# Kernel optimization log

Hardware: AMD Instinct MI355X
Metric: run time of the kernel (lower is better)

The kernel has to match this reference:

```python
import jax, jax.numpy as jnp
import numpy as np

C = 256       # in_channels
A = 6         # act_dim
B = 10000     # number of graphs (batch)
N = B * A     # total nodes
E = 960000    # number of edges
H = 32        # hidden_size


def setup_inputs() -> dict:
    key = jax.random.key(0)
    ks = jax.random.split(key, 20)
    s = 1.0 / np.sqrt(C)
    inp = {
        "state": jax.random.normal(ks[0], (N, C), jnp.float32),
        "edge_index": jax.random.randint(ks[1], (2, E), 0, N, jnp.int32),
        "action": jax.random.uniform(ks[2], (B, A), jnp.float32),
    }
    # GCNConv params (weight [C,C], bias [C]); conv4/conv5 exist but are unused by forward
    for i in range(5):
        inp[f"W{i+1}"] = jax.random.normal(ks[3 + i], (C, C), jnp.float32) * s
        inp[f"b{i+1}"] = jnp.zeros((C,), jnp.float32)
    D1 = 6 * C + 1
    inp["lin1_w"] = jax.random.normal(ks[10], (D1, H), jnp.float32) / np.sqrt(D1)
    inp["lin1_b"] = jnp.zeros((H,), jnp.float32)
    inp["lin2_w"] = jax.random.normal(ks[11], (H, H), jnp.float32) / np.sqrt(H)
    inp["lin2_b"] = jnp.zeros((H,), jnp.float32)
    inp["lin3_w"] = jax.random.normal(ks[12], (H, 1), jnp.float32) / np.sqrt(H)
    inp["lin3_b"] = jnp.zeros((1,), jnp.float32)
    return inp


def _gcn(x, W, b, src, dst, dinv):
    # PyG GCNConv: xW, then D^{-1/2}(A+I)D^{-1/2} aggregation, then bias.
    xw = x @ W                                    # [N, C]
    norm = dinv[src] * dinv[dst]                  # [E]
    agg = jax.ops.segment_sum(xw[src] * norm[:, None], dst, num_segments=N)
    agg = agg + xw * (dinv * dinv)[:, None]       # self-loop term
    return agg + b


def reference(state, edge_index, action,
              W1, b1, W2, b2, W3, b3, W4, b4, W5, b5,
              lin1_w, lin1_b, lin2_w, lin2_b, lin3_w, lin3_b):
    src, dst = edge_index[0], edge_index[1]
    # degree of A + I, computed at destination nodes (gcn_norm with self-loops)
    deg = jax.ops.segment_sum(jnp.ones((E,), state.dtype), dst, num_segments=N) + 1.0
    dinv = jax.lax.rsqrt(deg)

    o1 = jax.nn.relu(_gcn(state, W1, b1, src, dst, dinv))
    o2 = jax.nn.relu(_gcn(o1, W2, b2, src, dst, dinv))
    o3 = jax.nn.relu(_gcn(o2, W3, b3, src, dst, dinv))
    # NOTE: original forward reuses conv3 for layers 4 and 5 (replicated faithfully)
    o4 = jax.nn.relu(_gcn(o3, W3, b3, src, dst, dinv))
    o5 = jax.nn.relu(_gcn(o4, W3, b3, src, dst, dinv))

    r = lambda t: t.reshape(-1, A, C)             # [B, A, C]
    concat = jnp.concatenate(
        [r(o1), r(o2), r(o3), r(o4), r(o5), r(state), action[..., None]], axis=-1)
    x = jax.nn.relu(concat @ lin1_w + lin1_b)     # [B, A, H]
    x = jax.nn.relu(x @ lin2_w + lin2_b)
    x = jnp.sum(x, axis=1)                        # readout over act_dim
    x = (x @ lin3_w + lin3_b).squeeze(-1)         # [B]
    return x
```

## Files before the change

kernel.cpp:

```cpp
#include <hip/hip_runtime.h>
#include <hip/hip_fp16.h>

#define NNODES 60000
#define NEDGES 960000
#define NGRAPH 10000

struct __align__(16) H8 { __half2 h[4]; };
struct __align__(8)  H4 { __half2 h[2]; };

typedef _Float16 f16x8 __attribute__((ext_vector_type(8)));
typedef float f32x4 __attribute__((ext_vector_type(4)));

#define LDA 264


__global__ void count_deg_k(const int* __restrict__ ei, int* __restrict__ deg) {
  int e = blockIdx.x * blockDim.x + threadIdx.x;
  atomicAdd(&deg[ei[NEDGES + e]], 1);
}

__global__ void scan1_k(const int* __restrict__ deg, int* __restrict__ rs,
                        int* __restrict__ bsum, float* __restrict__ dinv) {
  __shared__ int s[256];
  int tid = threadIdx.x;
  int i = blockIdx.x * 256 + tid;
  int v = (i < NNODES) ? deg[i] : 0;
  if (i < NNODES) dinv[i] = rsqrtf((float)v + 1.0f);
  int x = v;
  s[tid] = x; __syncthreads();
  #pragma unroll
  for (int off = 1; off < 256; off <<= 1) {
    int t = (tid >= off) ? s[tid - off] : 0;
    __syncthreads();
    x += t; s[tid] = x; __syncthreads();
  }
  if (i < NNODES) rs[i] = x - v;
  if (tid == 255) bsum[blockIdx.x] = x;
}

__global__ void scan2_k(int* __restrict__ bsum, int nb) {
  __shared__ int s[256];
  int tid = threadIdx.x;
  int v = (tid < nb) ? bsum[tid] : 0;
  int x = v; s[tid] = x; __syncthreads();
  #pragma unroll
  for (int off = 1; off < 256; off <<= 1) {
    int t = (tid >= off) ? s[tid - off] : 0;
    __syncthreads();
    x += t; s[tid] = x; __syncthreads();
  }
  if (tid < nb) bsum[tid] = x - v;
}

__global__ void scan3_k(int* __restrict__ rs, const int* __restrict__ bsum) {
  int i = blockIdx.x * 256 + threadIdx.x;
  if (i < NNODES) rs[i] += bsum[blockIdx.x];
  if (i == 0) rs[NNODES] = NEDGES;
}

__global__ void scatter_k(const int* __restrict__ ei, const int* __restrict__ rs,
                          int* __restrict__ cursor, unsigned short* __restrict__ csr) {
  int e = blockIdx.x * blockDim.x + threadIdx.x;
  int s = ei[e], d = ei[NEDGES + e];
  int pos = rs[d] + atomicAdd(&cursor[d], 1);
  csr[pos] = (unsigned short)s;
}


__global__ void wpack_k(const float* __restrict__ W1, const float* __restrict__ W2,
                        const float* __restrict__ W3, __half* __restrict__ B1,
                        __half* __restrict__ B2, __half* __restrict__ B3) {
  int which = blockIdx.x >> 7;
  int c = blockIdx.x & 127;
  const float* W = which == 0 ? W1 : (which == 1 ? W2 : W3);
  __half* Bp = which == 0 ? B1 : (which == 1 ? B2 : B3);
  int kq = c >> 4, wcf = c & 15;
  int t = threadIdx.x;
  int l = t >> 2;
  int j0 = (t & 3) * 2;
  int li = l & 15, lg = l >> 4;
  int n = wcf * 16 + li;
  int k = kq * 32 + lg * 8 + j0;
  __half2 v;
  v.x = __float2half_rn(W[(size_t)k * 256 + n]);
  v.y = __float2half_rn(W[(size_t)(k + 1) * 256 + n]);
  *reinterpret_cast<__half2*>(Bp + (size_t)c * 512 + 2 * t) = v;
}

__global__ void lwpack_k(const float* __restrict__ l1w, __half* __restrict__ Pp) {
  int b = blockIdx.x;
  int l = b >> 4, cp = b & 15;
  int kq = cp >> 1, hh = cp & 1;
  int t = threadIdx.x;
  int ln = t >> 2;
  int j0 = (t & 3) * 2;
  int li = ln & 15, lg = ln >> 4;
  int dim = hh * 16 + li;
  int k = kq * 32 + lg * 8 + j0;
  __half2 v;
  v.x = __float2half_rn(l1w[((size_t)l * 256 + k) * 32 + dim]);
  v.y = __float2half_rn(l1w[((size_t)l * 256 + k + 1) * 32 + dim]);
  *reinterpret_cast<__half2*>(Pp + (size_t)b * 512 + 2 * t) = v;
}


__device__ __forceinline__ void gemm_body32(
    _Float16 (*As)[LDA], int m0, int nh, int tid,
    const __half* __restrict__ Bp, const __half* __restrict__ Pp,
    const float* __restrict__ dinv, __half* __restrict__ Y,
    float* __restrict__ part) {
  const int lane = tid & 63;
  const int wid = tid >> 6;
  const int wr2 = wid >> 1, wcl = wid & 1;
  const int li = lane & 15, lg = lane >> 4;

  f32x4 acc[4];
  #pragma unroll
  for (int j = 0; j < 4; ++j) acc[j] = (f32x4){0.f, 0.f, 0.f, 0.f};
  f32x4 p = (f32x4){0.f, 0.f, 0.f, 0.f};

  const __half* bwave = Bp + (size_t)(nh * 8 + wcl * 4) * 512 + lane * 8;
  const __half* pbase = Pp + (size_t)wcl * 512 + lane * 8;

  #pragma unroll
  for (int kq = 0; kq < 8; ++kq) {
    int k0 = kq * 32;
    f16x8 a = *reinterpret_cast<const f16x8*>(&As[wr2 * 16 + li][k0 + lg * 8]);
    f16x8 b0 = *reinterpret_cast<const f16x8*>(bwave + ((size_t)kq * 16 + 0) * 512);
    f16x8 b1 = *reinterpret_cast<const f16x8*>(bwave + ((size_t)kq * 16 + 1) * 512);
    f16x8 b2 = *reinterpret_cast<const f16x8*>(bwave + ((size_t)kq * 16 + 2) * 512);
    f16x8 b3 = *reinterpret_cast<const f16x8*>(bwave + ((size_t)kq * 16 + 3) * 512);
    acc[0] = __builtin_amdgcn_mfma_f32_16x16x32_f16(b0, a, acc[0], 0, 0, 0);
    acc[1] = __builtin_amdgcn_mfma_f32_16x16x32_f16(b1, a, acc[1], 0, 0, 0);
    acc[2] = __builtin_amdgcn_mfma_f32_16x16x32_f16(b2, a, acc[2], 0, 0, 0);
    acc[3] = __builtin_amdgcn_mfma_f32_16x16x32_f16(b3, a, acc[3], 0, 0, 0);
    if (nh == 0) {
      f16x8 bp = *reinterpret_cast<const f16x8*>(pbase + (size_t)kq * 2 * 512);
      p = __builtin_amdgcn_mfma_f32_16x16x32_f16(bp, a, p, 0, 0, 0);
    }
  }

  __syncthreads();

  {
    int row = wr2 * 16 + li;
    int r = m0 + row;
    float dv = dinv[r];
    #pragma unroll
    for (int cf = 0; cf < 4; ++cf) {
      int col = wcl * 64 + cf * 16 + lg * 4;
      H4 o;
      o.h[0].x = __float2half_rn(acc[cf][0] * dv);
      o.h[0].y = __float2half_rn(acc[cf][1] * dv);
      o.h[1].x = __float2half_rn(acc[cf][2] * dv);
      o.h[1].y = __float2half_rn(acc[cf][3] * dv);
      *reinterpret_cast<H4*>(&As[row][col]) = o;
    }
    if (nh == 0) {
      float4 v;
      v.x = p[0]; v.y = p[1]; v.z = p[2]; v.w = p[3];
      *reinterpret_cast<float4*>(part + (size_t)r * 32 + wcl * 16 + lg * 4) = v;
    }
  }

  __syncthreads();

  #pragma unroll
  for (int l = 0; l < 2; ++l) {
    int f = l * 256 + tid;
    int row = f >> 4, c8 = (f & 15) * 8;
    *reinterpret_cast<H8*>(Y + (size_t)(m0 + row) * 256 + nh * 128 + c8) =
        *reinterpret_cast<const H8*>(&As[row][c8]);
  }
}


__launch_bounds__(256, 6)
__global__ void gemm0_k(const float* __restrict__ Xf, const __half* __restrict__ Bp,
                        const float* __restrict__ dinv, __half* __restrict__ Y,
                        const __half* __restrict__ Pp, float* __restrict__ part) {
  __shared__ _Float16 As[32][LDA];
  const int tid = threadIdx.x;
  const int m0 = (blockIdx.x >> 1) * 32;
  const int nh = blockIdx.x & 1;
  #pragma unroll
  for (int l = 0; l < 4; ++l) {
    int f = l * 256 + tid;
    int row = f >> 5, c8 = (f & 31) * 8;
    const float* src = Xf + (size_t)(m0 + row) * 256 + c8;
    float4 u = *reinterpret_cast<const float4*>(src);
    float4 v = *reinterpret_cast<const float4*>(src + 4);
    H8 o;
    o.h[0].x = __float2half_rn(u.x); o.h[0].y = __float2half_rn(u.y);
    o.h[1].x = __float2half_rn(u.z); o.h[1].y = __float2half_rn(u.w);
    o.h[2].x = __float2half_rn(v.x); o.h[2].y = __float2half_rn(v.y);
    o.h[3].x = __float2half_rn(v.z); o.h[3].y = __float2half_rn(v.w);
    *reinterpret_cast<H8*>(&As[row][c8]) = o;
  }
  __syncthreads();
  gemm_body32(As, m0, nh, tid, Bp, Pp, dinv, Y, part);
}


__launch_bounds__(256, 6)
__global__ void gemm_k(const __half* __restrict__ Xh, const __half* __restrict__ Bp,
                       const float* __restrict__ dinv, __half* __restrict__ Y,
                       const __half* __restrict__ Pp, float* __restrict__ part) {
  __shared__ _Float16 As[32][LDA];
  const int tid = threadIdx.x;
  const int m0 = (blockIdx.x >> 1) * 32;
  const int nh = blockIdx.x & 1;
  #pragma unroll
  for (int l = 0; l < 4; ++l) {
    int f = l * 256 + tid;
    int row = f >> 5, c8 = (f & 31) * 8;
    *reinterpret_cast<H8*>(&As[row][c8]) =
        *reinterpret_cast<const H8*>(Xh + (size_t)(m0 + row) * 256 + c8);
  }
  __syncthreads();
  gemm_body32(As, m0, nh, tid, Bp, Pp, dinv, Y, part);
}


__launch_bounds__(256, 4)
__global__ void proj_k(const __half* __restrict__ Xh, const __half* __restrict__ Pp,
                       float* __restrict__ part) {
  __shared__ _Float16 As[64][LDA];
  const int tid = threadIdx.x;
  const int m0 = blockIdx.x * 64;
  #pragma unroll
  for (int l = 0; l < 8; ++l) {
    int f = l * 256 + tid;
    int row = f >> 5, c8 = (f & 31) * 8;
    *reinterpret_cast<H8*>(&As[row][c8]) =
        *reinterpret_cast<const H8*>(Xh + (size_t)(m0 + row) * 256 + c8);
  }
  __syncthreads();

  const int lane = tid & 63;
  const int wid = tid >> 6;
  const int li = lane & 15, lg = lane >> 4;
  const __half* pbase = Pp + lane * 8;

  f32x4 p0 = (f32x4){0.f, 0.f, 0.f, 0.f};
  f32x4 p1 = (f32x4){0.f, 0.f, 0.f, 0.f};
  #pragma unroll
  for (int kq = 0; kq < 8; ++kq) {
    int k0 = kq * 32;
    f16x8 ap = *reinterpret_cast<const f16x8*>(&As[wid * 16 + li][k0 + lg * 8]);
    f16x8 bp0 = *reinterpret_cast<const f16x8*>(pbase + ((size_t)kq * 2 + 0) * 512);
    f16x8 bp1 = *reinterpret_cast<const f16x8*>(pbase + ((size_t)kq * 2 + 1) * 512);
    p0 = __builtin_amdgcn_mfma_f32_16x16x32_f16(bp0, ap, p0, 0, 0, 0);
    p1 = __builtin_amdgcn_mfma_f32_16x16x32_f16(bp1, ap, p1, 0, 0, 0);
  }
  int pr = m0 + wid * 16 + li;
  {
    float4 v0, v1;
    v0.x = p0[0]; v0.y = p0[1]; v0.z = p0[2]; v0.w = p0[3];
    v1.x = p1[0]; v1.y = p1[1]; v1.z = p1[2]; v1.w = p1[3];
    *reinterpret_cast<float4*>(part + (size_t)pr * 32 + lg * 4) = v0;
    *reinterpret_cast<float4*>(part + (size_t)pr * 32 + 16 + lg * 4) = v1;
  }
}


__device__ inline void addH8(float* acc, const H8& v) {
  #pragma unroll
  for (int q = 0; q < 4; ++q) {
    acc[q * 2 + 0] += __low2float(v.h[q]);
    acc[q * 2 + 1] += __high2float(v.h[q]);
  }
}

__global__ void gather_k(const __half* __restrict__ ysh, const int* __restrict__ rs,
                         const unsigned short* __restrict__ csr, const float* __restrict__ dinv,
                         const float* __restrict__ bias, __half* __restrict__ out) {
  int tid = threadIdx.x;
  int lane = tid & 63;
  int wave = (blockIdx.x * blockDim.x + tid) >> 6;
  int d = wave * 2 + (lane >> 5);
  int c8 = (lane & 31) * 8;

  float acc[8];
  H8 self = *reinterpret_cast<const H8*>(ysh + (size_t)d * 256 + c8);
  #pragma unroll
  for (int q = 0; q < 4; ++q) {
    acc[q * 2 + 0] = __low2float(self.h[q]);
    acc[q * 2 + 1] = __high2float(self.h[q]);
  }

  int e = rs[d], end = rs[d + 1];
  for (; e + 3 < end; e += 4) {
    int s0 = csr[e], s1 = csr[e + 1], s2 = csr[e + 2], s3 = csr[e + 3];
    H8 v0 = *reinterpret_cast<const H8*>(ysh + (size_t)s0 * 256 + c8);
    H8 v1 = *reinterpret_cast<const H8*>(ysh + (size_t)s1 * 256 + c8);
    H8 v2 = *reinterpret_cast<const H8*>(ysh + (size_t)s2 * 256 + c8);
    H8 v3 = *reinterpret_cast<const H8*>(ysh + (size_t)s3 * 256 + c8);
    addH8(acc, v0);
    addH8(acc, v1);
    addH8(acc, v2);
    addH8(acc, v3);
  }
  for (; e < end; ++e) {
    int s0 = csr[e];
    H8 v0 = *reinterpret_cast<const H8*>(ysh + (size_t)s0 * 256 + c8);
    addH8(acc, v0);
  }

  float dv = dinv[d];
  float4 b0 = *reinterpret_cast<const float4*>(bias + c8);
  float4 b1 = *reinterpret_cast<const float4*>(bias + c8 + 4);
  float r0 = fmaxf(acc[0] * dv + b0.x, 0.f);
  float r1 = fmaxf(acc[1] * dv + b0.y, 0.f);
  float r2 = fmaxf(acc[2] * dv + b0.z, 0.f);
  float r3 = fmaxf(acc[3] * dv + b0.w, 0.f);
  float r4 = fmaxf(acc[4] * dv + b1.x, 0.f);
  float r5 = fmaxf(acc[5] * dv + b1.y, 0.f);
  float r6 = fmaxf(acc[6] * dv + b1.z, 0.f);
  float r7 = fmaxf(acc[7] * dv + b1.w, 0.f);
  H8 o;
  o.h[0].x = __float2half_rn(r0); o.h[0].y = __float2half_rn(r1);
  o.h[1].x = __float2half_rn(r2); o.h[1].y = __float2half_rn(r3);
  o.h[2].x = __float2half_rn(r4); o.h[2].y = __float2half_rn(r5);
  o.h[3].x = __float2half_rn(r6); o.h[3].y = __float2half_rn(r7);
  *reinterpret_cast<H8*>(out + (size_t)d * 256 + c8) = o;
}


__launch_bounds__(192)
__global__ void mlpfinal_k(const float* __restrict__ p0, const float* __restrict__ p1,
                           const float* __restrict__ p2, const float* __restrict__ p3,
                           const float* __restrict__ p4, const float* __restrict__ p5,
                           const float* __restrict__ action, const float* __restrict__ l1wlast,
                           const float* __restrict__ l1b, const float* __restrict__ l2w,
                           const float* __restrict__ l2b, const float* __restrict__ l3w,
                           const float* __restrict__ l3b, float* __restrict__ out) {
  __shared__ float w2s[1024];
  __shared__ float h1s[6][33];
  __shared__ float red[3];
  int tid = threadIdx.x;
  for (int i = tid; i < 1024; i += 192) w2s[i] = l2w[i];
  int a = tid >> 5, dim = tid & 31;
  int n = blockIdx.x * 6 + a;
  int idx = n * 32 + dim;
  float h1 = l1b[dim] + action[n] * l1wlast[dim]
           + p0[idx] + p1[idx] + p2[idx] + p3[idx] + p4[idx] + p5[idx];
  h1s[a][dim] = fmaxf(h1, 0.f);
  __syncthreads();
  float acc = l2b[dim];
  #pragma unroll
  for (int k = 0; k < 32; ++k) acc += h1s[a][k] * w2s[k * 32 + dim];
  float v = fmaxf(acc, 0.f) * l3w[dim];
  #pragma unroll
  for (int off = 32; off; off >>= 1) v += __shfl_down(v, off, 64);
  int lane = tid & 63, wave = tid >> 6;
  if (lane == 0) red[wave] = v;
  __syncthreads();
  if (tid == 0) out[blockIdx.x] = red[0] + red[1] + red[2] + l3b[0];
}


extern "C" void kernel_launch(void* const* d_in, const int* in_sizes, int n_in,
                              void* d_out, int out_size, void* d_ws, size_t ws_size,
                              hipStream_t stream) {
  const float* state  = (const float*)d_in[0];
  const int*   ei     = (const int*)d_in[1];
  const float* action = (const float*)d_in[2];
  const float* W1 = (const float*)d_in[3];
  const float* b1 = (const float*)d_in[4];
  const float* W2 = (const float*)d_in[5];
  const float* b2 = (const float*)d_in[6];
  const float* W3 = (const float*)d_in[7];
  const float* b3 = (const float*)d_in[8];
  const float* l1w = (const float*)d_in[13];
  const float* l1b = (const float*)d_in[14];
  const float* l2w = (const float*)d_in[15];
  const float* l2b = (const float*)d_in[16];
  const float* l3w = (const float*)d_in[17];
  const float* l3b = (const float*)d_in[18];
  float* out = (float*)d_out;

  char* base = (char*)d_ws;
  size_t off = 0;
  auto carve = [&](size_t bytes) {
    char* q = base + off;
    off += (bytes + 255) & ~(size_t)255;
    return q;
  };
  __half* ysh   = (__half*)carve((size_t)NNODES * 256 * 2);
  __half* obufh = (__half*)carve((size_t)NNODES * 256 * 2);
  __half* Bp1   = (__half*)carve(128 * 512 * 2);
  __half* Bp2   = (__half*)carve(128 * 512 * 2);
  __half* Bp3   = (__half*)carve(128 * 512 * 2);
  __half* Pp    = (__half*)carve(96 * 512 * 2);
  float* parts[6];
  for (int i = 0; i < 6; ++i) parts[i] = (float*)carve((size_t)NNODES * 32 * 4);
  float* dinv  = (float*)carve(NNODES * 4);
  char*  zbase = (char*)carve(0);
  int*   deg   = (int*)carve(NNODES * 4);
  int*   cursor= (int*)carve(NNODES * 4);
  size_t zlen  = (size_t)((char*)carve(0) - zbase);
  int*   rs    = (int*)carve((NNODES + 1) * 4);
  unsigned short* csr = (unsigned short*)carve((size_t)NEDGES * 2);
  int*   bsum  = (int*)carve(256 * 4);

  hipMemsetAsync(zbase, 0, zlen, stream);

  wpack_k<<<128 * 3, 256, 0, stream>>>(W1, W2, W3, Bp1, Bp2, Bp3);
  lwpack_k<<<96, 256, 0, stream>>>(l1w, Pp);

  count_deg_k<<<NEDGES / 256, 256, 0, stream>>>(ei, deg);
  int nb = (NNODES + 255) / 256;
  scan1_k<<<nb, 256, 0, stream>>>(deg, rs, bsum, dinv);
  scan2_k<<<1, 256, 0, stream>>>(bsum, nb);
  scan3_k<<<nb, 256, 0, stream>>>(rs, bsum);
  scatter_k<<<NEDGES / 256, 256, 0, stream>>>(ei, rs, cursor, csr);

  int gblocks = (NNODES / 32) * 2;
  const __half* Bps[5] = {Bp1, Bp2, Bp3, Bp3, Bp3};
  const float*  bs[5]  = {b1, b2, b3, b3, b3};

  gemm0_k<<<gblocks, 256, 0, stream>>>(state, Bp1, dinv, ysh,
                                       Pp + (size_t)5 * 16 * 512, parts[5]);
  for (int layer = 1; layer < 5; ++layer) {
    gather_k<<<NNODES / 8, 256, 0, stream>>>(ysh, rs, csr, dinv, bs[layer - 1], obufh);
    gemm_k<<<gblocks, 256, 0, stream>>>(obufh, Bps[layer], dinv, ysh,
                                        Pp + (size_t)(layer - 1) * 16 * 512, parts[layer - 1]);
  }
  gather_k<<<NNODES / 8, 256, 0, stream>>>(ysh, rs, csr, dinv, b3, obufh);
  proj_k<<<NNODES / 64, 256, 0, stream>>>(obufh, Pp + (size_t)4 * 16 * 512, parts[4]);

  mlpfinal_k<<<NGRAPH, 192, 0, stream>>>(parts[0], parts[1], parts[2], parts[3], parts[4],
                                         parts[5], action, l1w + 1536 * 32, l1b, l2w, l2b,
                                         l3w, l3b, out);
}
```

Baseline: 642.2 us.

## Compute full 256-wide GEMM per block, fuse prep kernels, fold last projection into MLP

Each GEMM block now computes all 256 output columns for its 32 rows instead of splitting the columns across two blocks. This halves the A-tile loads and removes the duplicate projection branch, at the cost of more accumulator registers and lower occupancy. The weight-packing kernels and the memset are merged into one prep kernel that also zeroes the degree and cursor arrays. The separate proj_k launch is removed, and the layer-5 projection is computed inside mlpfinal_k as a scalar dot product over fp16 o5 read from global memory, which trades an MFMA kernel for per-thread scalar FMAs.

New measurement: 653.6 us. Within noise of the previous version (+1.8%).

```diff
diff --git a/kernel.cpp b/kernel.cpp
--- a/kernel.cpp
+++ b/kernel.cpp
@@ -67,45 +67,50 @@
 }
 
 
-__global__ void wpack_k(const float* __restrict__ W1, const float* __restrict__ W2,
-                        const float* __restrict__ W3, __half* __restrict__ B1,
-                        __half* __restrict__ B2, __half* __restrict__ B3) {
-  int which = blockIdx.x >> 7;
-  int c = blockIdx.x & 127;
-  const float* W = which == 0 ? W1 : (which == 1 ? W2 : W3);
-  __half* Bp = which == 0 ? B1 : (which == 1 ? B2 : B3);
-  int kq = c >> 4, wcf = c & 15;
+__global__ void prep_k(const float* __restrict__ W1, const float* __restrict__ W2,
+                       const float* __restrict__ W3, const float* __restrict__ l1w,
+                       __half* __restrict__ B1, __half* __restrict__ B2,
+                       __half* __restrict__ B3, __half* __restrict__ Pp,
+                       int* __restrict__ deg, int* __restrict__ cursor) {
+  int bid = blockIdx.x;
   int t = threadIdx.x;
-  int l = t >> 2;
-  int j0 = (t & 3) * 2;
-  int li = l & 15, lg = l >> 4;
-  int n = wcf * 16 + li;
-  int k = kq * 32 + lg * 8 + j0;
-  __half2 v;
-  v.x = __float2half_rn(W[(size_t)k * 256 + n]);
-  v.y = __float2half_rn(W[(size_t)(k + 1) * 256 + n]);
-  *reinterpret_cast<__half2*>(Bp + (size_t)c * 512 + 2 * t) = v;
-}
-
-__global__ void lwpack_k(const float* __restrict__ l1w, __half* __restrict__ Pp) {
-  int b = blockIdx.x;
-  int l = b >> 4, cp = b & 15;
-  int kq = cp >> 1, hh = cp & 1;
-  int t = threadIdx.x;
-  int ln = t >> 2;
-  int j0 = (t & 3) * 2;
-  int li = ln & 15, lg = ln >> 4;
-  int dim = hh * 16 + li;
-  int k = kq * 32 + lg * 8 + j0;
-  __half2 v;
-  v.x = __float2half_rn(l1w[((size_t)l * 256 + k) * 32 + dim]);
-  v.y = __float2half_rn(l1w[((size_t)l * 256 + k + 1) * 32 + dim]);
-  *reinterpret_cast<__half2*>(Pp + (size_t)b * 512 + 2 * t) = v;
-}
-
-
-__device__ __forceinline__ void gemm_body32(
-    _Float16 (*As)[LDA], int m0, int nh, int tid,
+  if (bid < 384) {
+    int which = bid >> 7;
+    int c = bid & 127;
+    const float* W = which == 0 ? W1 : (which == 1 ? W2 : W3);
+    __half* Bp = which == 0 ? B1 : (which == 1 ? B2 : B3);
+    int kq = c >> 4, wcf = c & 15;
+    int l = t >> 2;
+    int j0 = (t & 3) * 2;
+    int li = l & 15, lg = l >> 4;
+    int n = wcf * 16 + li;
+    int k = kq * 32 + lg * 8 + j0;
+    __half2 v;
+    v.x = __float2half_rn(W[(size_t)k * 256 + n]);
+    v.y = __float2half_rn(W[(size_t)(k + 1) * 256 + n]);
+    *reinterpret_cast<__half2*>(Bp + (size_t)c * 512 + 2 * t) = v;
+  } else {
+    int b = bid - 384;
+    int l = b >> 4, cp = b & 15;
+    int kq = cp >> 1, hh = cp & 1;
+    int ln = t >> 2;
+    int j0 = (t & 3) * 2;
+    int li = ln & 15, lg = ln >> 4;
+    int dim = hh * 16 + li;
+    int k = kq * 32 + lg * 8 + j0;
+    __half2 v;
+    v.x = __float2half_rn(l1w[((size_t)l * 256 + k) * 32 + dim]);
+    v.y = __float2half_rn(l1w[((size_t)l * 256 + k + 1) * 32 + dim]);
+    *reinterpret_cast<__half2*>(Pp + (size_t)b * 512 + 2 * t) = v;
+  }
+  int z = bid * 256 + t;
+  if (z < NNODES) deg[z] = 0;
+  else if (z < 2 * NNODES) cursor[z - NNODES] = 0;
+}
+
+
+__device__ __forceinline__ void gemm_body256(
+    _Float16 (*As)[LDA], int m0, int tid,
     const __half* __restrict__ Bp, const __half* __restrict__ Pp,
     const float* __restrict__ dinv, __half* __restrict__ Y,
     float* __restrict__ part) {
@@ -114,27 +119,38 @@
   const int wr2 = wid >> 1, wcl = wid & 1;
   const int li = lane & 15, lg = lane >> 4;
 
-  f32x4 acc[4];
-  #pragma unroll
-  for (int j = 0; j < 4; ++j) acc[j] = (f32x4){0.f, 0.f, 0.f, 0.f};
+  f32x4 acc[8];
+  #pragma unroll
+  for (int j = 0; j < 8; ++j) acc[j] = (f32x4){0.f, 0.f, 0.f, 0.f};
   f32x4 p = (f32x4){0.f, 0.f, 0.f, 0.f};
 
-  const __half* bwave = Bp + (size_t)(nh * 8 + wcl * 4) * 512 + lane * 8;
+  const __half* bwave = Bp + (size_t)(wcl * 8) * 512 + lane * 8;
   const __half* pbase = Pp + (size_t)wcl * 512 + lane * 8;
 
   #pragma unroll
   for (int kq = 0; kq < 8; ++kq) {
-    int k0 = kq * 32;
-    f16x8 a = *reinterpret_cast<const f16x8*>(&As[wr2 * 16 + li][k0 + lg * 8]);
-    f16x8 b0 = *reinterpret_cast<const f16x8*>(bwave + ((size_t)kq * 16 + 0) * 512);
-    f16x8 b1 = *reinterpret_cast<const f16x8*>(bwave + ((size_t)kq * 16 + 1) * 512);
-    f16x8 b2 = *reinterpret_cast<const f16x8*>(bwave + ((size_t)kq * 16 + 2) * 512);
-    f16x8 b3 = *reinterpret_cast<const f16x8*>(bwave + ((size_t)kq * 16 + 3) * 512);
-    acc[0] = __builtin_amdgcn_mfma_f32_16x16x32_f16(b0, a, acc[0], 0, 0, 0);
-    acc[1] = __builtin_amdgcn_mfma_f32_16x16x32_f16(b1, a, acc[1], 0, 0, 0);
-    acc[2] = __builtin_amdgcn_mfma_f32_16x16x32_f16(b2, a, acc[2], 0, 0, 0);
-    acc[3] = __builtin_amdgcn_mfma_f32_16x16x32_f16(b3, a, acc[3], 0, 0, 0);
-    if (nh == 0) {
+    f16x8 a = *reinterpret_cast<const f16x8*>(&As[wr2 * 16 + li][kq * 32 + lg * 8]);
+    {
+      f16x8 b0 = *reinterpret_cast<const f16x8*>(bwave + ((size_t)kq * 16 + 0) * 512);
+      f16x8 b1 = *reinterpret_cast<const f16x8*>(bwave + ((size_t)kq * 16 + 1) * 512);
+      f16x8 b2 = *reinterpret_cast<const f16x8*>(bwave + ((size_t)kq * 16 + 2) * 512);
+      f16x8 b3 = *reinterpret_cast<const f16x8*>(bwave + ((size_t)kq * 16 + 3) * 512);
+      acc[0] = __builtin_amdgcn_mfma_f32_16x16x32_f16(b0, a, acc[0], 0, 0, 0);
+      acc[1] = __builtin_amdgcn_mfma_f32_16x16x32_f16(b1, a, acc[1], 0, 0, 0);
+      acc[2] = __builtin_amdgcn_mfma_f32_16x16x32_f16(b2, a, acc[2], 0, 0, 0);
+      acc[3] = __builtin_amdgcn_mfma_f32_16x16x32_f16(b3, a, acc[3], 0, 0, 0);
+    }
+    {
+      f16x8 b4 = *reinterpret_cast<const f16x8*>(bwave + ((size_t)kq * 16 + 4) * 512);
+      f16x8 b5 = *reinterpret_cast<const f16x8*>(bwave + ((size_t)kq * 16 + 5) * 512);
+      f16x8 b6 = *reinterpret_cast<const f16x8*>(bwave + ((size_t)kq * 16 + 6) * 512);
+      f16x8 b7 = *reinterpret_cast<const f16x8*>(bwave + ((size_t)kq * 16 + 7) * 512);
+      acc[4] = __builtin_amdgcn_mfma_f32_16x16x32_f16(b4, a, acc[4], 0, 0, 0);
+      acc[5] = __builtin_amdgcn_mfma_f32_16x16x32_f16(b5, a, acc[5], 0, 0, 0);
+      acc[6] = __builtin_amdgcn_mfma_f32_16x16x32_f16(b6, a, acc[6], 0, 0, 0);
+      acc[7] = __builtin_amdgcn_mfma_f32_16x16x32_f16(b7, a, acc[7], 0, 0, 0);
+    }
+    {
       f16x8 bp = *reinterpret_cast<const f16x8*>(pbase + (size_t)kq * 2 * 512);
       p = __builtin_amdgcn_mfma_f32_16x16x32_f16(bp, a, p, 0, 0, 0);
     }
@@ -147,8 +163,8 @@
     int r = m0 + row;
     float dv = dinv[r];
     #pragma unroll
-    for (int cf = 0; cf < 4; ++cf) {
-      int col = wcl * 64 + cf * 16 + lg * 4;
+    for (int cf = 0; cf < 8; ++cf) {
+      int col = wcl * 128 + cf * 16 + lg * 4;
       H4 o;
       o.h[0].x = __float2half_rn(acc[cf][0] * dv);
       o.h[0].y = __float2half_rn(acc[cf][1] * dv);
@@ -156,33 +172,30 @@
       o.h[1].y = __float2half_rn(acc[cf][3] * dv);
       *reinterpret_cast<H4*>(&As[row][col]) = o;
     }
-    if (nh == 0) {
-      float4 v;
-      v.x = p[0]; v.y = p[1]; v.z = p[2]; v.w = p[3];
-      *reinterpret_cast<float4*>(part + (size_t)r * 32 + wcl * 16 + lg * 4) = v;
-    }
-  }
-
-  __syncthreads();
-
-  #pragma unroll
-  for (int l = 0; l < 2; ++l) {
+    float4 v;
+    v.x = p[0]; v.y = p[1]; v.z = p[2]; v.w = p[3];
+    *reinterpret_cast<float4*>(part + (size_t)r * 32 + wcl * 16 + lg * 4) = v;
+  }
+
+  __syncthreads();
+
+  #pragma unroll
+  for (int l = 0; l < 4; ++l) {
     int f = l * 256 + tid;
-    int row = f >> 4, c8 = (f & 15) * 8;
-    *reinterpret_cast<H8*>(Y + (size_t)(m0 + row) * 256 + nh * 128 + c8) =
+    int row = f >> 5, c8 = (f & 31) * 8;
+    *reinterpret_cast<H8*>(Y + (size_t)(m0 + row) * 256 + c8) =
         *reinterpret_cast<const H8*>(&As[row][c8]);
   }
 }
 
 
-__launch_bounds__(256, 6)
+__launch_bounds__(256, 5)
 __global__ void gemm0_k(const float* __restrict__ Xf, const __half* __restrict__ Bp,
                         const float* __restrict__ dinv, __half* __restrict__ Y,
                         const __half* __restrict__ Pp, float* __restrict__ part) {
   __shared__ _Float16 As[32][LDA];
   const int tid = threadIdx.x;
-  const int m0 = (blockIdx.x >> 1) * 32;
-  const int nh = blockIdx.x & 1;
+  const int m0 = blockIdx.x * 32;
   #pragma unroll
   for (int l = 0; l < 4; ++l) {
     int f = l * 256 + tid;
@@ -198,18 +211,17 @@
     *reinterpret_cast<H8*>(&As[row][c8]) = o;
   }
   __syncthreads();
-  gemm_body32(As, m0, nh, tid, Bp, Pp, dinv, Y, part);
-}
-
-
-__launch_bounds__(256, 6)
+  gemm_body256(As, m0, tid, Bp, Pp, dinv, Y, part);
+}
+
+
+__launch_bounds__(256, 5)
 __global__ void gemm_k(const __half* __restrict__ Xh, const __half* __restrict__ Bp,
                        const float* __restrict__ dinv, __half* __restrict__ Y,
                        const __half* __restrict__ Pp, float* __restrict__ part) {
   __shared__ _Float16 As[32][LDA];
   const int tid = threadIdx.x;
-  const int m0 = (blockIdx.x >> 1) * 32;
-  const int nh = blockIdx.x & 1;
+  const int m0 = blockIdx.x * 32;
   #pragma unroll
   for (int l = 0; l < 4; ++l) {
     int f = l * 256 + tid;
@@ -218,49 +230,7 @@
         *reinterpret_cast<const H8*>(Xh + (size_t)(m0 + row) * 256 + c8);
   }
   __syncthreads();
-  gemm_body32(As, m0, nh, tid, Bp, Pp, dinv, Y, part);
-}
-
-
-__launch_bounds__(256, 4)
-__global__ void proj_k(const __half* __restrict__ Xh, const __half* __restrict__ Pp,
-                       float* __restrict__ part) {
-  __shared__ _Float16 As[64][LDA];
-  const int tid = threadIdx.x;
-  const int m0 = blockIdx.x * 64;
-  #pragma unroll
-  for (int l = 0; l < 8; ++l) {
-    int f = l * 256 + tid;
-    int row = f >> 5, c8 = (f & 31) * 8;
-    *reinterpret_cast<H8*>(&As[row][c8]) =
-        *reinterpret_cast<const H8*>(Xh + (size_t)(m0 + row) * 256 + c8);
-  }
-  __syncthreads();
-
-  const int lane = tid & 63;
-  const int wid = tid >> 6;
-  const int li = lane & 15, lg = lane >> 4;
-  const __half* pbase = Pp + lane * 8;
-
-  f32x4 p0 = (f32x4){0.f, 0.f, 0.f, 0.f};
-  f32x4 p1 = (f32x4){0.f, 0.f, 0.f, 0.f};
-  #pragma unroll
-  for (int kq = 0; kq < 8; ++kq) {
-    int k0 = kq * 32;
-    f16x8 ap = *reinterpret_cast<const f16x8*>(&As[wid * 16 + li][k0 + lg * 8]);
-    f16x8 bp0 = *reinterpret_cast<const f16x8*>(pbase + ((size_t)kq * 2 + 0) * 512);
-    f16x8 bp1 = *reinterpret_cast<const f16x8*>(pbase + ((size_t)kq * 2 + 1) * 512);
-    p0 = __builtin_amdgcn_mfma_f32_16x16x32_f16(bp0, ap, p0, 0, 0, 0);
-    p1 = __builtin_amdgcn_mfma_f32_16x16x32_f16(bp1, ap, p1, 0, 0, 0);
-  }
-  int pr = m0 + wid * 16 + li;
-  {
-    float4 v0, v1;
-    v0.x = p0[0]; v0.y = p0[1]; v0.z = p0[2]; v0.w = p0[3];
-    v1.x = p1[0]; v1.y = p1[1]; v1.z = p1[2]; v1.w = p1[3];
-    *reinterpret_cast<float4*>(part + (size_t)pr * 32 + lg * 4) = v0;
-    *reinterpret_cast<float4*>(part + (size_t)pr * 32 + 16 + lg * 4) = v1;
-  }
+  gemm_body256(As, m0, tid, Bp, Pp, dinv, Y, part);
 }
 
 
@@ -330,21 +300,33 @@
 __launch_bounds__(192)
 __global__ void mlpfinal_k(const float* __restrict__ p0, const float* __restrict__ p1,
                            const float* __restrict__ p2, const float* __restrict__ p3,
-                           const float* __restrict__ p4, const float* __restrict__ p5,
+                           const float* __restrict__ p5, const __half* __restrict__ o5h,
+                           const float* __restrict__ lw4,
                            const float* __restrict__ action, const float* __restrict__ l1wlast,
                            const float* __restrict__ l1b, const float* __restrict__ l2w,
                            const float* __restrict__ l2b, const float* __restrict__ l3w,
                            const float* __restrict__ l3b, float* __restrict__ out) {
   __shared__ float w2s[1024];
+  __shared__ __half o5s[6][256];
   __shared__ float h1s[6][33];
   __shared__ float red[3];
   int tid = threadIdx.x;
   for (int i = tid; i < 1024; i += 192) w2s[i] = l2w[i];
+  {
+    int row = tid >> 5, c8 = (tid & 31) * 8;
+    *reinterpret_cast<H8*>(&o5s[row][c8]) =
+        *reinterpret_cast<const H8*>(o5h + ((size_t)blockIdx.x * 6 + row) * 256 + c8);
+  }
+  __syncthreads();
   int a = tid >> 5, dim = tid & 31;
   int n = blockIdx.x * 6 + a;
   int idx = n * 32 + dim;
+  float p4 = 0.f;
+  #pragma unroll 8
+  for (int k = 0; k < 256; ++k)
+    p4 += __half2float(o5s[a][k]) * lw4[k * 32 + dim];
   float h1 = l1b[dim] + action[n] * l1wlast[dim]
-           + p0[idx] + p1[idx] + p2[idx] + p3[idx] + p4[idx] + p5[idx];
+           + p0[idx] + p1[idx] + p2[idx] + p3[idx] + p4 + p5[idx];
   h1s[a][dim] = fmaxf(h1, 0.f);
   __syncthreads();
   float acc = l2b[dim];
@@ -396,18 +378,13 @@
   float* parts[6];
   for (int i = 0; i < 6; ++i) parts[i] = (float*)carve((size_t)NNODES * 32 * 4);
   float* dinv  = (float*)carve(NNODES * 4);
-  char*  zbase = (char*)carve(0);
   int*   deg   = (int*)carve(NNODES * 4);
   int*   cursor= (int*)carve(NNODES * 4);
-  size_t zlen  = (size_t)((char*)carve(0) - zbase);
   int*   rs    = (int*)carve((NNODES + 1) * 4);
   unsigned short* csr = (unsigned short*)carve((size_t)NEDGES * 2);
   int*   bsum  = (int*)carve(256 * 4);
 
-  hipMemsetAsync(zbase, 0, zlen, stream);
-
-  wpack_k<<<128 * 3, 256, 0, stream>>>(W1, W2, W3, Bp1, Bp2, Bp3);
-  lwpack_k<<<96, 256, 0, stream>>>(l1w, Pp);
+  prep_k<<<480, 256, 0, stream>>>(W1, W2, W3, l1w, Bp1, Bp2, Bp3, Pp, deg, cursor);
 
   count_deg_k<<<NEDGES / 256, 256, 0, stream>>>(ei, deg);
   int nb = (NNODES + 255) / 256;
@@ -416,7 +393,7 @@
   scan3_k<<<nb, 256, 0, stream>>>(rs, bsum);
   scatter_k<<<NEDGES / 256, 256, 0, stream>>>(ei, rs, cursor, csr);
 
-  int gblocks = (NNODES / 32) * 2;
+  int gblocks = NNODES / 32;
   const __half* Bps[5] = {Bp1, Bp2, Bp3, Bp3, Bp3};
   const float*  bs[5]  = {b1, b2, b3, b3, b3};
 
@@ -428,9 +405,8 @@
                                         Pp + (size_t)(layer - 1) * 16 * 512, parts[layer - 1]);
   }
   gather_k<<<NNODES / 8, 256, 0, stream>>>(ysh, rs, csr, dinv, b3, obufh);
-  proj_k<<<NNODES / 64, 256, 0, stream>>>(obufh, Pp + (size_t)4 * 16 * 512, parts[4]);
-
-  mlpfinal_k<<<NGRAPH, 192, 0, stream>>>(parts[0], parts[1], parts[2], parts[3], parts[4],
-                                         parts[5], action, l1w + 1536 * 32, l1b, l2w, l2b,
-                                         l3w, l3b, out);
-}
+
+  mlpfinal_k<<<NGRAPH, 192, 0, stream>>>(parts[0], parts[1], parts[2], parts[3], parts[5],
+                                         obufh, l1w + 1024 * 32, action, l1w + 1536 * 32,
+                                         l1b, l2w, l2b, l3w, l3b, out);
+}
```
